# Performance work log

Measured on AMD Instinct MI355X. Metric: run time of the kernel, lower is better.

Reference implementation:

```python
import jax, jax.numpy as jnp
import numpy as np

NEG_SLOPE = 0.2


def setup_inputs() -> dict:
    key = jax.random.key(0)
    k1, k2, k3 = jax.random.split(key, 3)
    B, N, IN, OUT, C = 2048, 256, 256, 256, 1024
    x = jax.random.normal(k1, (B, N, IN), dtype=jnp.float32)
    indices = jax.random.randint(k2, (B,), 0, C)
    # kaiming-uniform-like init for weight
    bound = float(np.sqrt(6.0 / IN))
    weight = jax.random.uniform(k3, (C, IN, OUT), dtype=jnp.float32, minval=-bound, maxval=bound)
    bias = jnp.zeros((1, 1, OUT), dtype=jnp.float32)
    return {"x": x, "indices": indices, "weight": weight, "bias": bias}


def reference(x, indices, weight, bias):
    # gather per-batch weight tiles: [B, IN, OUT], then batched matmul
    w = weight[indices]                      # [B, IN, OUT]
    out = jnp.einsum('bni,bio->bno', x, w)   # [B, N, OUT]
    out = out + bias[0]                      # bias[0] is [1, OUT], broadcasts
    return jnp.where(out >= 0, out, NEG_SLOPE * out)  # LeakyReLU(0.2)
```

## Files before the change

kernel.cpp:

```cpp
#include <hip/hip_runtime.h>
#include <hip/hip_bf16.h>


#define K_DIM 256
#define O_DIM 256
#define BK 32

typedef __attribute__((ext_vector_type(8))) __bf16 bf16x8;
typedef __attribute__((ext_vector_type(4))) float f32x4;
typedef __attribute__((ext_vector_type(4))) unsigned int u32x4;
typedef __attribute__((ext_vector_type(2))) unsigned int u32x2;

__device__ __forceinline__ f32x4 MFMA(u32x4 a, u32x4 b, f32x4 c) {
    return __builtin_amdgcn_mfma_f32_16x16x32_bf16(
        __builtin_bit_cast(bf16x8, a), __builtin_bit_cast(bf16x8, b), c, 0, 0, 0);
}

__device__ __forceinline__ unsigned pk2(float a, float b) {
    __hip_bfloat16 ha = __float2bfloat16(a);
    __hip_bfloat16 hb = __float2bfloat16(b);
    unsigned short sa, sb;
    __builtin_memcpy(&sa, &ha, 2);
    __builtin_memcpy(&sb, &hb, 2);
    return (unsigned)sa | ((unsigned)sb << 16);
}

__device__ __forceinline__ int bbyte(int o, int p) {
    const int rp  = o >> 1;
    const int raw = ((o & 1) << 2) | (p >> 3);
    const int key = (rp ^ (o >> 4)) & 7;
    return rp * 128 + ((raw ^ key) << 4) + ((p & 7) << 1);
}

__global__ __launch_bounds__(256) void argemm_kernel(
    const float* __restrict__ x,
    const int* __restrict__ idx,
    const float* __restrict__ w,
    const float* __restrict__ bias,
    float* __restrict__ out)
{
    __shared__ __align__(16) char lds[65536];

    const int tid = threadIdx.x;
    const int l   = tid & 63;
    const int wid = tid >> 6;
    const int wr  = wid >> 1;
    const int wc  = wid & 1;

    const unsigned bid     = blockIdx.x;
    const unsigned chunk   = gridDim.x >> 3;
    const unsigned logical = (bid & 7u) * chunk + (bid >> 3);
    const int b  = (int)(logical >> 2);
    const int n0 = (int)(logical & 3u) * 64;

    const int g = l >> 4;
    const int i = l & 15;

    const int c = idx[b];
    const float* xb = x + (size_t)b * (256 * 256);
    const float* wb = w + (size_t)c * (256 * 256);

    const int q   = tid & 63;
    const int oct = tid >> 6;
    const float* wp = wb + (size_t)(oct * 8) * O_DIM + q * 4;
    int bW[4];
#pragma unroll
    for (int j = 0; j < 4; ++j)
        bW[j] = bbyte(q * 4 + j, oct * 8);

    int bR[8];
#pragma unroll
    for (int n = 0; n < 8; ++n)
        bR[n] = bbyte(wc * 128 + n * 16 + i, g * 8);
    int aRow[2], aKey[2];
#pragma unroll
    for (int m = 0; m < 2; ++m) {
        const int r = wr * 32 + m * 16 + i;
        aRow[m] = r * 512;
        aKey[m] = r & 31;
    }

    f32x4 rb[2][8];

    auto issueB = [&](int t, int s) {
#pragma unroll
        for (int e = 0; e < 8; ++e)
            rb[s][e] = *(const f32x4*)(wp + (size_t)(t * BK + e) * O_DIM);
    };
    auto flushB = [&](int T, int s) {
        char* base = (char*)lds + 32768 + (T & 1) * 16384;
#pragma unroll
        for (int j = 0; j < 4; ++j) {
            u32x4 pq;
            pq.x = pk2(rb[s][0][j], rb[s][1][j]);
            pq.y = pk2(rb[s][2][j], rb[s][3][j]);
            pq.z = pk2(rb[s][4][j], rb[s][5][j]);
            pq.w = pk2(rb[s][6][j], rb[s][7][j]);
            *(u32x4*)(base + bW[j]) = pq;
        }
    };

    issueB(0, 0);
    __builtin_amdgcn_sched_barrier(0);
    issueB(1, 1);
    __builtin_amdgcn_sched_barrier(0);

    {
        const float* xw = xb + (n0 + wid * 16) * 256 + l * 4;
        const int csw = l >> 1;
        const int sub = (l & 1) * 8;
        f32x4 xa[8];
#pragma unroll
        for (int s2 = 0; s2 < 2; ++s2) {
#pragma unroll
            for (int j = 0; j < 8; ++j)
                xa[j] = __builtin_nontemporal_load(
                    (const f32x4*)(xw + (s2 * 8 + j) * 256));
            __builtin_amdgcn_sched_barrier(0);
#pragma unroll
            for (int j = 0; j < 8; ++j) {
                const int r = wid * 16 + s2 * 8 + j;
                u32x2 p;
                p.x = pk2(xa[j].x, xa[j].y);
                p.y = pk2(xa[j].z, xa[j].w);
                *(u32x2*)((char*)lds + r * 512 + ((csw ^ (r & 31)) << 4) + sub) = p;
            }
        }
    }

    flushB(0, 0);
    issueB(2, 0);
    __builtin_amdgcn_sched_barrier(0);
    asm volatile("s_waitcnt lgkmcnt(0)" ::: "memory");
    __builtin_amdgcn_sched_barrier(0);
    __builtin_amdgcn_s_barrier();

    f32x4 acc[2][8];
#pragma unroll
    for (int m = 0; m < 2; ++m)
#pragma unroll
        for (int n = 0; n < 8; ++n)
            acc[m][n] = (f32x4){0.f, 0.f, 0.f, 0.f};

#pragma unroll
    for (int t = 0; t < 8; ++t) {
        const char* bbuf = (const char*)lds + 32768 + (t & 1) * 16384;

        u32x4 af[2];
#pragma unroll
        for (int m = 0; m < 2; ++m)
            af[m] = *(const u32x4*)((const char*)lds + aRow[m]
                                    + (((t * 4 + g) ^ aKey[m]) << 4));
#pragma unroll
        for (int n = 0; n < 8; ++n) {
            const u32x4 bq = *(const u32x4*)(bbuf + bR[n]);
#pragma unroll
            for (int m = 0; m < 2; ++m)
                acc[m][n] = MFMA(af[m], bq, acc[m][n]);
        }

        if (t < 7) {
            flushB(t + 1, (t + 1) & 1);
            if (t < 5) {
                issueB(t + 3, (t + 1) & 1);
                __builtin_amdgcn_sched_barrier(0);
            }
            asm volatile("s_waitcnt lgkmcnt(0)" ::: "memory");
            __builtin_amdgcn_sched_barrier(0);
            __builtin_amdgcn_s_barrier();
        }
    }

    float biasf[8];
#pragma unroll
    for (int n = 0; n < 8; ++n)
        biasf[n] = bias[wc * 128 + n * 16 + i];

    float* ob = out + (size_t)b * (256 * 256);
#pragma unroll
    for (int m = 0; m < 2; ++m) {
#pragma unroll
        for (int r = 0; r < 4; ++r) {
            const int row = n0 + wr * 32 + m * 16 + g * 4 + r;
#pragma unroll
            for (int n = 0; n < 8; ++n) {
                float v = acc[m][n][r] + biasf[n];
                v = (v >= 0.f) ? v : 0.2f * v;
                __builtin_nontemporal_store(
                    v, &ob[row * 256 + wc * 128 + n * 16 + i]);
            }
        }
    }
}

extern "C" void kernel_launch(void* const* d_in, const int* in_sizes, int n_in,
                              void* d_out, int out_size, void* d_ws, size_t ws_size,
                              hipStream_t stream) {
    const float* x    = (const float*)d_in[0];
    const int*   idx  = (const int*)d_in[1];
    const float* w    = (const float*)d_in[2];
    const float* bias = (const float*)d_in[3];
    float*       out  = (float*)d_out;
    (void)d_ws; (void)ws_size; (void)n_in; (void)out_size;

    const int B = in_sizes[1];
    dim3 grid((unsigned)(B * 4)), block(256);
    hipLaunchKernelGGL(argemm_kernel, grid, block, 0, stream, x, idx, w, bias, out);
}
```

Measured before the change: 248.3 us.

## Double rows per block to 128 with 512 threads and single-buffered B tile

Each workgroup now covers 128 rows of x with 8 waves, each wave owning 16 rows and all 256 output columns, instead of 64 rows with 4 waves. The intent is to load and convert each gathered weight tile once per 128 rows rather than once per 64, halving weight reads and bf16 conversion work per batch. The B tile in LDS becomes a single buffer refilled each K step, with one step of register prefetch. That costs an extra barrier per iteration and shallower prefetch. Total LDS rises to 80 KB per block, which limits how many blocks fit on a CU.

```diff
diff --git a/kernel.cpp b/kernel.cpp
--- a/kernel.cpp
+++ b/kernel.cpp
@@ -2,14 +2,14 @@
 #include <hip/hip_bf16.h>
 
 
-#define K_DIM 256
-#define O_DIM 256
 #define BK 32
 
 typedef __attribute__((ext_vector_type(8))) __bf16 bf16x8;
 typedef __attribute__((ext_vector_type(4))) float f32x4;
 typedef __attribute__((ext_vector_type(4))) unsigned int u32x4;
 typedef __attribute__((ext_vector_type(2))) unsigned int u32x2;
+
+#define B_LDS 65536
 
 __device__ __forceinline__ f32x4 MFMA(u32x4 a, u32x4 b, f32x4 c) {
     return __builtin_amdgcn_mfma_f32_16x16x32_bf16(
@@ -32,29 +32,26 @@
     return rp * 128 + ((raw ^ key) << 4) + ((p & 7) << 1);
 }
 
-__global__ __launch_bounds__(256) void argemm_kernel(
+__global__ __launch_bounds__(512, 4) void argemm_kernel(
     const float* __restrict__ x,
     const int* __restrict__ idx,
     const float* __restrict__ w,
     const float* __restrict__ bias,
     float* __restrict__ out)
 {
-    __shared__ __align__(16) char lds[65536];
+    __shared__ __align__(16) char lds[81920];
 
     const int tid = threadIdx.x;
     const int l   = tid & 63;
     const int wid = tid >> 6;
-    const int wr  = wid >> 1;
-    const int wc  = wid & 1;
+    const int g   = l >> 4;
+    const int i   = l & 15;
 
     const unsigned bid     = blockIdx.x;
     const unsigned chunk   = gridDim.x >> 3;
     const unsigned logical = (bid & 7u) * chunk + (bid >> 3);
-    const int b  = (int)(logical >> 2);
-    const int n0 = (int)(logical & 3u) * 64;
-
-    const int g = l >> 4;
-    const int i = l & 15;
+    const int n0 = (int)(logical & 1u) * 128;
+    const int b  = (int)(logical >> 1);
 
     const int c = idx[b];
     const float* xb = x + (size_t)b * (256 * 256);
@@ -62,47 +59,36 @@
 
     const int q   = tid & 63;
     const int oct = tid >> 6;
-    const float* wp = wb + (size_t)(oct * 8) * O_DIM + q * 4;
+    const float* wp = wb + (size_t)(oct * 4) * 256 + q * 4;
     int bW[4];
 #pragma unroll
     for (int j = 0; j < 4; ++j)
-        bW[j] = bbyte(q * 4 + j, oct * 8);
+        bW[j] = B_LDS + bbyte(q * 4 + j, oct * 4);
 
-    int bR[8];
+    int bR[16];
 #pragma unroll
-    for (int n = 0; n < 8; ++n)
-        bR[n] = bbyte(wc * 128 + n * 16 + i, g * 8);
-    int aRow[2], aKey[2];
+    for (int n = 0; n < 16; ++n)
+        bR[n] = B_LDS + bbyte(n * 16 + i, g * 8);
+    const int aRow = (wid * 16 + i) * 512;
+    const int aKey = (wid * 16 + i) & 31;
+
+    f32x4 rb[4];
+    auto issueB = [&](int t) {
 #pragma unroll
-    for (int m = 0; m < 2; ++m) {
-        const int r = wr * 32 + m * 16 + i;
-        aRow[m] = r * 512;
-        aKey[m] = r & 31;
-    }
-
-    f32x4 rb[2][8];
-
-    auto issueB = [&](int t, int s) {
-#pragma unroll
-        for (int e = 0; e < 8; ++e)
-            rb[s][e] = *(const f32x4*)(wp + (size_t)(t * BK + e) * O_DIM);
+        for (int e = 0; e < 4; ++e)
+            rb[e] = *(const f32x4*)(wp + (size_t)t * (BK * 256) + e * 256);
     };
-    auto flushB = [&](int T, int s) {
-        char* base = (char*)lds + 32768 + (T & 1) * 16384;
+    auto flushB = [&]() {
 #pragma unroll
         for (int j = 0; j < 4; ++j) {
-            u32x4 pq;
-            pq.x = pk2(rb[s][0][j], rb[s][1][j]);
-            pq.y = pk2(rb[s][2][j], rb[s][3][j]);
-            pq.z = pk2(rb[s][4][j], rb[s][5][j]);
-            pq.w = pk2(rb[s][6][j], rb[s][7][j]);
-            *(u32x4*)(base + bW[j]) = pq;
+            u32x2 pr;
+            pr.x = pk2(rb[0][j], rb[1][j]);
+            pr.y = pk2(rb[2][j], rb[3][j]);
+            *(u32x2*)((char*)lds + bW[j]) = pr;
         }
     };
 
-    issueB(0, 0);
-    __builtin_amdgcn_sched_barrier(0);
-    issueB(1, 1);
+    issueB(0);
     __builtin_amdgcn_sched_barrier(0);
 
     {
@@ -127,68 +113,56 @@
             }
         }
     }
-
-    flushB(0, 0);
-    issueB(2, 0);
-    __builtin_amdgcn_sched_barrier(0);
+    flushB();
     asm volatile("s_waitcnt lgkmcnt(0)" ::: "memory");
     __builtin_amdgcn_sched_barrier(0);
     __builtin_amdgcn_s_barrier();
 
-    f32x4 acc[2][8];
+    f32x4 acc[16];
 #pragma unroll
-    for (int m = 0; m < 2; ++m)
-#pragma unroll
-        for (int n = 0; n < 8; ++n)
-            acc[m][n] = (f32x4){0.f, 0.f, 0.f, 0.f};
+    for (int n = 0; n < 16; ++n)
+        acc[n] = (f32x4){0.f, 0.f, 0.f, 0.f};
 
 #pragma unroll
     for (int t = 0; t < 8; ++t) {
-        const char* bbuf = (const char*)lds + 32768 + (t & 1) * 16384;
+        if (t < 7) {
+            issueB(t + 1);
+            __builtin_amdgcn_sched_barrier(0);
+        }
 
-        u32x4 af[2];
+        const u32x4 af = *(const u32x4*)((const char*)lds + aRow
+                                         + (((t * 4 + g) ^ aKey) << 4));
 #pragma unroll
-        for (int m = 0; m < 2; ++m)
-            af[m] = *(const u32x4*)((const char*)lds + aRow[m]
-                                    + (((t * 4 + g) ^ aKey[m]) << 4));
-#pragma unroll
-        for (int n = 0; n < 8; ++n) {
-            const u32x4 bq = *(const u32x4*)(bbuf + bR[n]);
-#pragma unroll
-            for (int m = 0; m < 2; ++m)
-                acc[m][n] = MFMA(af[m], bq, acc[m][n]);
+        for (int n = 0; n < 16; ++n) {
+            const u32x4 bq = *(const u32x4*)((const char*)lds + bR[n]);
+            acc[n] = MFMA(af, bq, acc[n]);
         }
 
         if (t < 7) {
-            flushB(t + 1, (t + 1) & 1);
-            if (t < 5) {
-                issueB(t + 3, (t + 1) & 1);
-                __builtin_amdgcn_sched_barrier(0);
-            }
+            asm volatile("s_waitcnt lgkmcnt(0)" ::: "memory");
+            __builtin_amdgcn_sched_barrier(0);
+            __builtin_amdgcn_s_barrier();
+            flushB();
             asm volatile("s_waitcnt lgkmcnt(0)" ::: "memory");
             __builtin_amdgcn_sched_barrier(0);
             __builtin_amdgcn_s_barrier();
         }
     }
 
-    float biasf[8];
+    float biasf[16];
 #pragma unroll
-    for (int n = 0; n < 8; ++n)
-        biasf[n] = bias[wc * 128 + n * 16 + i];
+    for (int n = 0; n < 16; ++n)
+        biasf[n] = bias[n * 16 + i];
 
     float* ob = out + (size_t)b * (256 * 256);
 #pragma unroll
-    for (int m = 0; m < 2; ++m) {
+    for (int r = 0; r < 4; ++r) {
+        const int row = n0 + wid * 16 + g * 4 + r;
 #pragma unroll
-        for (int r = 0; r < 4; ++r) {
-            const int row = n0 + wr * 32 + m * 16 + g * 4 + r;
-#pragma unroll
-            for (int n = 0; n < 8; ++n) {
-                float v = acc[m][n][r] + biasf[n];
-                v = (v >= 0.f) ? v : 0.2f * v;
-                __builtin_nontemporal_store(
-                    v, &ob[row * 256 + wc * 128 + n * 16 + i]);
-            }
+        for (int n = 0; n < 16; ++n) {
+            float v = acc[n][r] + biasf[n];
+            v = (v >= 0.f) ? v : 0.2f * v;
+            __builtin_nontemporal_store(v, &ob[row * 256 + n * 16 + i]);
         }
     }
 }
@@ -204,6 +178,6 @@
     (void)d_ws; (void)ws_size; (void)n_in; (void)out_size;
 
     const int B = in_sizes[1];
-    dim3 grid((unsigned)(B * 4)), block(256);
+    dim3 grid((unsigned)(B * 2)), block(512);
     hipLaunchKernelGGL(argemm_kernel, grid, block, 0, stream, x, idx, w, bias, out);
 }
```

After: 292.5 us. +17.8%, slower.

## Halve rows per block to cut LDS and raise occupancy

Applied to the files above, without the earlier changes.

Each block now computes 32 rows instead of 64 for a given batch, with twice as many blocks. The A region of LDS shrinks so total shared memory drops from 64KB to 48KB, and launch bounds request 3 blocks per CU. This aims to hide latency with more resident waves. In exchange, each weight tile is loaded and converted to bf16 by twice as many blocks, raising L2 traffic and conversion work per output.

```diff
diff --git a/kernel.cpp b/kernel.cpp
--- a/kernel.cpp
+++ b/kernel.cpp
@@ -2,14 +2,14 @@
 #include <hip/hip_bf16.h>
 
 
-#define K_DIM 256
-#define O_DIM 256
 #define BK 32
 
 typedef __attribute__((ext_vector_type(8))) __bf16 bf16x8;
 typedef __attribute__((ext_vector_type(4))) float f32x4;
 typedef __attribute__((ext_vector_type(4))) unsigned int u32x4;
 typedef __attribute__((ext_vector_type(2))) unsigned int u32x2;
+
+#define B_LDS 16384
 
 __device__ __forceinline__ f32x4 MFMA(u32x4 a, u32x4 b, f32x4 c) {
     return __builtin_amdgcn_mfma_f32_16x16x32_bf16(
@@ -32,14 +32,14 @@
     return rp * 128 + ((raw ^ key) << 4) + ((p & 7) << 1);
 }
 
-__global__ __launch_bounds__(256) void argemm_kernel(
+__global__ __launch_bounds__(256, 3) void argemm_kernel(
     const float* __restrict__ x,
     const int* __restrict__ idx,
     const float* __restrict__ w,
     const float* __restrict__ bias,
     float* __restrict__ out)
 {
-    __shared__ __align__(16) char lds[65536];
+    __shared__ __align__(16) char lds[49152];
 
     const int tid = threadIdx.x;
     const int l   = tid & 63;
@@ -50,8 +50,8 @@
     const unsigned bid     = blockIdx.x;
     const unsigned chunk   = gridDim.x >> 3;
     const unsigned logical = (bid & 7u) * chunk + (bid >> 3);
-    const int b  = (int)(logical >> 2);
-    const int n0 = (int)(logical & 3u) * 64;
+    const int b  = (int)(logical >> 3);
+    const int n0 = (int)(logical & 7u) * 32;
 
     const int g = l >> 4;
     const int i = l & 15;
@@ -62,7 +62,7 @@
 
     const int q   = tid & 63;
     const int oct = tid >> 6;
-    const float* wp = wb + (size_t)(oct * 8) * O_DIM + q * 4;
+    const float* wp = wb + (size_t)(oct * 8) * 256 + q * 4;
     int bW[4];
 #pragma unroll
     for (int j = 0; j < 4; ++j)
@@ -72,23 +72,18 @@
 #pragma unroll
     for (int n = 0; n < 8; ++n)
         bR[n] = bbyte(wc * 128 + n * 16 + i, g * 8);
-    int aRow[2], aKey[2];
-#pragma unroll
-    for (int m = 0; m < 2; ++m) {
-        const int r = wr * 32 + m * 16 + i;
-        aRow[m] = r * 512;
-        aKey[m] = r & 31;
-    }
+    const int aRow = (wr * 16 + i) * 512;
+    const int aKey = (wr * 16 + i) & 31;
 
     f32x4 rb[2][8];
 
     auto issueB = [&](int t, int s) {
 #pragma unroll
         for (int e = 0; e < 8; ++e)
-            rb[s][e] = *(const f32x4*)(wp + (size_t)(t * BK + e) * O_DIM);
+            rb[s][e] = *(const f32x4*)(wp + (size_t)(t * BK + e) * 256);
     };
     auto flushB = [&](int T, int s) {
-        char* base = (char*)lds + 32768 + (T & 1) * 16384;
+        char* base = (char*)lds + B_LDS + (T & 1) * 16384;
 #pragma unroll
         for (int j = 0; j < 4; ++j) {
             u32x4 pq;
@@ -106,25 +101,21 @@
     __builtin_amdgcn_sched_barrier(0);
 
     {
-        const float* xw = xb + (n0 + wid * 16) * 256 + l * 4;
+        const float* xw = xb + (n0 + wid * 8) * 256 + l * 4;
         const int csw = l >> 1;
         const int sub = (l & 1) * 8;
         f32x4 xa[8];
 #pragma unroll
-        for (int s2 = 0; s2 < 2; ++s2) {
+        for (int j = 0; j < 8; ++j)
+            xa[j] = __builtin_nontemporal_load((const f32x4*)(xw + j * 256));
+        __builtin_amdgcn_sched_barrier(0);
 #pragma unroll
-            for (int j = 0; j < 8; ++j)
-                xa[j] = __builtin_nontemporal_load(
-                    (const f32x4*)(xw + (s2 * 8 + j) * 256));
-            __builtin_amdgcn_sched_barrier(0);
-#pragma unroll
-            for (int j = 0; j < 8; ++j) {
-                const int r = wid * 16 + s2 * 8 + j;
-                u32x2 p;
-                p.x = pk2(xa[j].x, xa[j].y);
-                p.y = pk2(xa[j].z, xa[j].w);
-                *(u32x2*)((char*)lds + r * 512 + ((csw ^ (r & 31)) << 4) + sub) = p;
-            }
+        for (int j = 0; j < 8; ++j) {
+            const int r = wid * 8 + j;
+            u32x2 p;
+            p.x = pk2(xa[j].x, xa[j].y);
+            p.y = pk2(xa[j].z, xa[j].w);
+            *(u32x2*)((char*)lds + r * 512 + ((csw ^ (r & 31)) << 4) + sub) = p;
         }
     }
 
@@ -135,28 +126,21 @@
     __builtin_amdgcn_sched_barrier(0);
     __builtin_amdgcn_s_barrier();
 
-    f32x4 acc[2][8];
+    f32x4 acc[8];
 #pragma unroll
-    for (int m = 0; m < 2; ++m)
-#pragma unroll
-        for (int n = 0; n < 8; ++n)
-            acc[m][n] = (f32x4){0.f, 0.f, 0.f, 0.f};
+    for (int n = 0; n < 8; ++n)
+        acc[n] = (f32x4){0.f, 0.f, 0.f, 0.f};
 
 #pragma unroll
     for (int t = 0; t < 8; ++t) {
-        const char* bbuf = (const char*)lds + 32768 + (t & 1) * 16384;
+        const char* bbuf = (const char*)lds + B_LDS + (t & 1) * 16384;
 
-        u32x4 af[2];
-#pragma unroll
-        for (int m = 0; m < 2; ++m)
-            af[m] = *(const u32x4*)((const char*)lds + aRow[m]
-                                    + (((t * 4 + g) ^ aKey[m]) << 4));
+        const u32x4 af = *(const u32x4*)((const char*)lds + aRow
+                                         + (((t * 4 + g) ^ aKey) << 4));
 #pragma unroll
         for (int n = 0; n < 8; ++n) {
             const u32x4 bq = *(const u32x4*)(bbuf + bR[n]);
-#pragma unroll
-            for (int m = 0; m < 2; ++m)
-                acc[m][n] = MFMA(af[m], bq, acc[m][n]);
+            acc[n] = MFMA(af, bq, acc[n]);
         }
 
         if (t < 7) {
@@ -178,17 +162,13 @@
 
     float* ob = out + (size_t)b * (256 * 256);
 #pragma unroll
-    for (int m = 0; m < 2; ++m) {
+    for (int r = 0; r < 4; ++r) {
+        const int row = n0 + wr * 16 + g * 4 + r;
 #pragma unroll
-        for (int r = 0; r < 4; ++r) {
-            const int row = n0 + wr * 32 + m * 16 + g * 4 + r;
-#pragma unroll
-            for (int n = 0; n < 8; ++n) {
-                float v = acc[m][n][r] + biasf[n];
-                v = (v >= 0.f) ? v : 0.2f * v;
-                __builtin_nontemporal_store(
-                    v, &ob[row * 256 + wc * 128 + n * 16 + i]);
-            }
+        for (int n = 0; n < 8; ++n) {
+            float v = acc[n][r] + biasf[n];
+            v = (v >= 0.f) ? v : 0.2f * v;
+            __builtin_nontemporal_store(v, &ob[row * 256 + wc * 128 + n * 16 + i]);
         }
     }
 }
@@ -204,6 +184,6 @@
     (void)d_ws; (void)ws_size; (void)n_in; (void)out_size;
 
     const int B = in_sizes[1];
-    dim3 grid((unsigned)(B * 4)), block(256);
+    dim3 grid((unsigned)(B * 8)), block(256);
     hipLaunchKernelGGL(argemm_kernel, grid, block, 0, stream, x, idx, w, bias, out);
 }
```

Result: slower. 307.7 us (+23.9%).

## Make kernel persistent with 256 blocks and cross-tile prefetch of A and B

Applied to the files above, without the earlier changes.

The kernel moves from one block per 64-row tile (8192 blocks) to a persistent grid of 256 blocks, each looping over 32 consecutive tiles. The next tile's x rows are prefetched into a double-buffered A region of LDS, and the next tile's weight slices are prefetched during the current tile's last k-steps. This hides the prologue load latency and removes per-block launch and setup cost. In exchange LDS use grows to 96KB, which limits occupancy to one block per CU. The grid size is hard-coded to B=2048, and the fixed 256 blocks may not balance well across all CUs.

```diff
diff --git a/kernel.cpp b/kernel.cpp
--- a/kernel.cpp
+++ b/kernel.cpp
@@ -2,14 +2,14 @@
 #include <hip/hip_bf16.h>
 
 
-#define K_DIM 256
-#define O_DIM 256
 #define BK 32
 
 typedef __attribute__((ext_vector_type(8))) __bf16 bf16x8;
 typedef __attribute__((ext_vector_type(4))) float f32x4;
 typedef __attribute__((ext_vector_type(4))) unsigned int u32x4;
 typedef __attribute__((ext_vector_type(2))) unsigned int u32x2;
+
+#define B_LDS 65536
 
 __device__ __forceinline__ f32x4 MFMA(u32x4 a, u32x4 b, f32x4 c) {
     return __builtin_amdgcn_mfma_f32_16x16x32_bf16(
@@ -39,7 +39,7 @@
     const float* __restrict__ bias,
     float* __restrict__ out)
 {
-    __shared__ __align__(16) char lds[65536];
+    __shared__ __align__(16) char lds[98304];
 
     const int tid = threadIdx.x;
     const int l   = tid & 63;
@@ -47,22 +47,17 @@
     const int wr  = wid >> 1;
     const int wc  = wid & 1;
 
-    const unsigned bid     = blockIdx.x;
-    const unsigned chunk   = gridDim.x >> 3;
-    const unsigned logical = (bid & 7u) * chunk + (bid >> 3);
-    const int b  = (int)(logical >> 2);
-    const int n0 = (int)(logical & 3u) * 64;
+    const int p = (int)blockIdx.x;
 
     const int g = l >> 4;
     const int i = l & 15;
 
-    const int c = idx[b];
-    const float* xb = x + (size_t)b * (256 * 256);
-    const float* wb = w + (size_t)c * (256 * 256);
+    auto bOf  = [&](int j) { return (p * 32 + j) >> 2; };
+    auto n0Of = [&](int j) { return ((p * 32 + j) & 3) * 64; };
 
     const int q   = tid & 63;
     const int oct = tid >> 6;
-    const float* wp = wb + (size_t)(oct * 8) * O_DIM + q * 4;
+    const size_t wpoff = (size_t)(oct * 8) * 256 + q * 4;
     int bW[4];
 #pragma unroll
     for (int j = 0; j < 4; ++j)
@@ -79,16 +74,29 @@
         aRow[m] = r * 512;
         aKey[m] = r & 31;
     }
+    const int csw = l >> 1;
+    const int sub = (l & 1) * 8;
+
+    float biasf[8];
+#pragma unroll
+    for (int n = 0; n < 8; ++n)
+        biasf[n] = bias[wc * 128 + n * 16 + i];
+
+    const float* wp_cur  = w + (size_t)idx[bOf(0)] * 65536 + wpoff;
+    const float* wp_next = w + (size_t)idx[bOf(1)] * 65536 + wpoff;
+    const float* xg_next = x + (size_t)bOf(1) * 65536
+                           + (size_t)(n0Of(1) + wid * 16) * 256 + l * 4;
 
     f32x4 rb[2][8];
-
-    auto issueB = [&](int t, int s) {
+    f32x4 xa[4];
+
+    auto issueB = [&](const float* wp, int tt, int s) {
 #pragma unroll
         for (int e = 0; e < 8; ++e)
-            rb[s][e] = *(const f32x4*)(wp + (size_t)(t * BK + e) * O_DIM);
-    };
-    auto flushB = [&](int T, int s) {
-        char* base = (char*)lds + 32768 + (T & 1) * 16384;
+            rb[s][e] = *(const f32x4*)(wp + (size_t)(tt * BK + e) * 256);
+    };
+    auto flushB = [&](int s) {
+        char* base = (char*)lds + B_LDS + s * 16384;
 #pragma unroll
         for (int j = 0; j < 4; ++j) {
             u32x4 pq;
@@ -99,37 +107,50 @@
             *(u32x4*)(base + bW[j]) = pq;
         }
     };
-
-    issueB(0, 0);
-    __builtin_amdgcn_sched_barrier(0);
-    issueB(1, 1);
-    __builtin_amdgcn_sched_barrier(0);
-
+    auto issueA = [&](int k) {
+#pragma unroll
+        for (int j2 = 0; j2 < 4; ++j2)
+            xa[j2] = __builtin_nontemporal_load(
+                (const f32x4*)(xg_next + (k * 4 + j2) * 256));
+    };
+    auto flushA = [&](int k, char* An) {
+#pragma unroll
+        for (int j2 = 0; j2 < 4; ++j2) {
+            const int r = wid * 16 + k * 4 + j2;
+            u32x2 pr;
+            pr.x = pk2(xa[j2].x, xa[j2].y);
+            pr.y = pk2(xa[j2].z, xa[j2].w);
+            *(u32x2*)(An + r * 512 + ((csw ^ (r & 31)) << 4) + sub) = pr;
+        }
+    };
+
+    issueB(wp_cur, 0, 0);
+    __builtin_amdgcn_sched_barrier(0);
+    issueB(wp_cur, 1, 1);
+    __builtin_amdgcn_sched_barrier(0);
     {
-        const float* xw = xb + (n0 + wid * 16) * 256 + l * 4;
-        const int csw = l >> 1;
-        const int sub = (l & 1) * 8;
-        f32x4 xa[8];
+        const float* xw = x + (size_t)bOf(0) * 65536
+                          + (size_t)(n0Of(0) + wid * 16) * 256 + l * 4;
+        f32x4 t8[8];
 #pragma unroll
         for (int s2 = 0; s2 < 2; ++s2) {
 #pragma unroll
             for (int j = 0; j < 8; ++j)
-                xa[j] = __builtin_nontemporal_load(
+                t8[j] = __builtin_nontemporal_load(
                     (const f32x4*)(xw + (s2 * 8 + j) * 256));
             __builtin_amdgcn_sched_barrier(0);
 #pragma unroll
             for (int j = 0; j < 8; ++j) {
                 const int r = wid * 16 + s2 * 8 + j;
-                u32x2 p;
-                p.x = pk2(xa[j].x, xa[j].y);
-                p.y = pk2(xa[j].z, xa[j].w);
-                *(u32x2*)((char*)lds + r * 512 + ((csw ^ (r & 31)) << 4) + sub) = p;
+                u32x2 pr;
+                pr.x = pk2(t8[j].x, t8[j].y);
+                pr.y = pk2(t8[j].z, t8[j].w);
+                *(u32x2*)((char*)lds + r * 512 + ((csw ^ (r & 31)) << 4) + sub) = pr;
             }
         }
     }
-
-    flushB(0, 0);
-    issueB(2, 0);
+    flushB(0);
+    issueB(wp_cur, 2, 0);
     __builtin_amdgcn_sched_barrier(0);
     asm volatile("s_waitcnt lgkmcnt(0)" ::: "memory");
     __builtin_amdgcn_sched_barrier(0);
@@ -142,53 +163,81 @@
         for (int n = 0; n < 8; ++n)
             acc[m][n] = (f32x4){0.f, 0.f, 0.f, 0.f};
 
-#pragma unroll
-    for (int t = 0; t < 8; ++t) {
-        const char* bbuf = (const char*)lds + 32768 + (t & 1) * 16384;
-
-        u32x4 af[2];
-#pragma unroll
-        for (int m = 0; m < 2; ++m)
-            af[m] = *(const u32x4*)((const char*)lds + aRow[m]
-                                    + (((t * 4 + g) ^ aKey[m]) << 4));
-#pragma unroll
-        for (int n = 0; n < 8; ++n) {
-            const u32x4 bq = *(const u32x4*)(bbuf + bR[n]);
+    for (int j = 0; j < 32; ++j) {
+        char* Ac = (char*)lds + (j & 1) * 32768;
+        char* An = (char*)lds + ((j & 1) ^ 1) * 32768;
+        const bool haveNext = (j < 31);
+
+#pragma unroll
+        for (int t = 0; t < 8; ++t) {
+            const char* bbuf = (const char*)lds + B_LDS + (t & 1) * 16384;
+
+            u32x4 af[2];
 #pragma unroll
             for (int m = 0; m < 2; ++m)
-                acc[m][n] = MFMA(af[m], bq, acc[m][n]);
-        }
-
-        if (t < 7) {
-            flushB(t + 1, (t + 1) & 1);
-            if (t < 5) {
-                issueB(t + 3, (t + 1) & 1);
+                af[m] = *(const u32x4*)(Ac + aRow[m]
+                                        + (((t * 4 + g) ^ aKey[m]) << 4));
+#pragma unroll
+            for (int n = 0; n < 8; ++n) {
+                const u32x4 bq = *(const u32x4*)(bbuf + bR[n]);
+#pragma unroll
+                for (int m = 0; m < 2; ++m)
+                    acc[m][n] = MFMA(af[m], bq, acc[m][n]);
+            }
+
+            if (t < 7 || haveNext)
+                flushB((t + 1) & 1);
+            if (t < 5)
+                issueB(wp_cur, t + 3, (t + 1) & 1);
+            else if (haveNext)
+                issueB(wp_next, t - 5, (t + 1) & 1);
+            __builtin_amdgcn_sched_barrier(0);
+
+            if (haveNext) {
+                if (t == 2) flushA(0, An);
+                if (t == 4) flushA(1, An);
+                if (t == 6) flushA(2, An);
+                if (t == 7) flushA(3, An);
+                if (t == 0) issueA(0);
+                if (t == 2) issueA(1);
+                if (t == 4) issueA(2);
+                if (t == 6) issueA(3);
                 __builtin_amdgcn_sched_barrier(0);
             }
+
+            if (t == 7) {
+                const int n0 = n0Of(j);
+                float* ob = out + (size_t)bOf(j) * 65536;
+#pragma unroll
+                for (int m = 0; m < 2; ++m)
+#pragma unroll
+                    for (int r = 0; r < 4; ++r) {
+                        const int row = n0 + wr * 32 + m * 16 + g * 4 + r;
+#pragma unroll
+                        for (int n = 0; n < 8; ++n) {
+                            float v = acc[m][n][r] + biasf[n];
+                            v = (v >= 0.f) ? v : 0.2f * v;
+                            __builtin_nontemporal_store(
+                                v, &ob[row * 256 + wc * 128 + n * 16 + i]);
+                        }
+                    }
+#pragma unroll
+                for (int m = 0; m < 2; ++m)
+#pragma unroll
+                    for (int n = 0; n < 8; ++n)
+                        acc[m][n] = (f32x4){0.f, 0.f, 0.f, 0.f};
+            }
+
             asm volatile("s_waitcnt lgkmcnt(0)" ::: "memory");
             __builtin_amdgcn_sched_barrier(0);
             __builtin_amdgcn_s_barrier();
         }
-    }
-
-    float biasf[8];
-#pragma unroll
-    for (int n = 0; n < 8; ++n)
-        biasf[n] = bias[wc * 128 + n * 16 + i];
-
-    float* ob = out + (size_t)b * (256 * 256);
-#pragma unroll
-    for (int m = 0; m < 2; ++m) {
-#pragma unroll
-        for (int r = 0; r < 4; ++r) {
-            const int row = n0 + wr * 32 + m * 16 + g * 4 + r;
-#pragma unroll
-            for (int n = 0; n < 8; ++n) {
-                float v = acc[m][n][r] + biasf[n];
-                v = (v >= 0.f) ? v : 0.2f * v;
-                __builtin_nontemporal_store(
-                    v, &ob[row * 256 + wc * 128 + n * 16 + i]);
-            }
+
+        wp_cur = wp_next;
+        if (j + 2 < 32) {
+            wp_next = w + (size_t)idx[bOf(j + 2)] * 65536 + wpoff;
+            xg_next = x + (size_t)bOf(j + 2) * 65536
+                      + (size_t)(n0Of(j + 2) + wid * 16) * 256 + l * 4;
         }
     }
 }
@@ -203,7 +252,6 @@
     float*       out  = (float*)d_out;
     (void)d_ws; (void)ws_size; (void)n_in; (void)out_size;
 
-    const int B = in_sizes[1];
-    dim3 grid((unsigned)(B * 4)), block(256);
+    dim3 grid(256), block(256);
     hipLaunchKernelGGL(argemm_kernel, grid, block, 0, stream, x, idx, w, bias, out);
 }
```

Measured after the change: 492.4 us. 98.3% more time.
